# Performance work log

Hardware: AMD Instinct MI355X
Metric: run time of the kernel (lower is better)

Reference implementation:

```python
import jax, jax.numpy as jnp
import numpy as np

B, S, HID = 2, 2048, 2048
NH, NKV, HD = 16, 8, 128
EPS = 1e-6
THETA = 1e6
SCALE = HD ** -0.5


def setup_inputs() -> dict:
    key = jax.random.key(0)
    k0, k1, k2 = jax.random.split(key, 3)
    hidden_states = jax.random.normal(k0, (B, S, HID), dtype=jnp.float32) * 0.02
    # real RoPE tables (rotate-half convention, half-dim cos/sin)
    inv_freq = 1.0 / (THETA ** (jnp.arange(0, HD, 2, dtype=jnp.float32) / HD))
    freqs = jnp.outer(jnp.arange(S, dtype=jnp.float32), inv_freq)  # [S, HD//2]
    cos, sin = jnp.cos(freqs), jnp.sin(freqs)
    w_qkv = jax.random.normal(k1, ((NH + 2 * NKV) * HD, HID), dtype=jnp.float32) * 0.02
    q_norm_w = jnp.ones((HD,), dtype=jnp.float32)
    k_norm_w = jnp.ones((HD,), dtype=jnp.float32)
    w_o = jax.random.normal(k2, (HID, NH * HD), dtype=jnp.float32) * 0.02
    return {
        "hidden_states": hidden_states,
        "cos": cos,
        "sin": sin,
        "w_qkv": w_qkv,
        "q_norm_w": q_norm_w,
        "k_norm_w": k_norm_w,
        "w_o": w_o,
    }


def _rms_norm(x, w):
    # per-head RMSNorm over last dim (head_dim)
    var = jnp.mean(jnp.square(x), axis=-1, keepdims=True)
    return x * jax.lax.rsqrt(var + EPS) * w


def _rope(x, cos, sin):
    # x: [B, S, H, HD]; cos/sin: [S, HD//2]; rotate-half convention
    x1, x2 = x[..., : HD // 2], x[..., HD // 2 :]
    c = cos[None, :, None, :]
    s = sin[None, :, None, :]
    return jnp.concatenate([x1 * c - x2 * s, x2 * c + x1 * s], axis=-1)


def reference(hidden_states, cos, sin, w_qkv, q_norm_w, k_norm_w, w_o):
    # fused QKV projection
    qkv = jnp.einsum("bsh,oh->bso", hidden_states, w_qkv)
    q, k, v = jnp.split(qkv, [NH * HD, NH * HD + NKV * HD], axis=-1)
    q = q.reshape(B, S, NH, HD)
    k = k.reshape(B, S, NKV, HD)
    v = v.reshape(B, S, NKV, HD)
    # per-head QK RMSNorm, then RoPE
    q = _rope(_rms_norm(q, q_norm_w), cos, sin)
    k = _rope(_rms_norm(k, k_norm_w), cos, sin)
    # GQA: repeat KV heads across query groups
    groups = NH // NKV
    k = jnp.repeat(k, groups, axis=2)  # [B, S, NH, HD]
    v = jnp.repeat(v, groups, axis=2)
    # causal attention (prefill, full window)
    scores = jnp.einsum("bqhd,bkhd->bhqk", q, k) * SCALE
    causal = jnp.tril(jnp.ones((S, S), dtype=bool))
    scores = jnp.where(causal[None, None], scores, jnp.finfo(scores.dtype).min)
    probs = jax.nn.softmax(scores, axis=-1)
    attn = jnp.einsum("bhqk,bkhd->bqhd", probs, v).reshape(B, S, NH * HD)
    return jnp.einsum("bso,ho->bsh", attn, w_o)
```

## Files before the change

### kernel.cpp

```cpp
#include <hip/hip_runtime.h>
#include <stdint.h>
#include <stddef.h>

typedef __attribute__((ext_vector_type(8))) short bf16x8;
typedef __attribute__((ext_vector_type(4))) float f32x4;

#define B_ 2
#define S_ 2048
#define HID_ 2048
#define NH_ 16
#define NKV_ 8
#define HD_ 128
#define SCALE_ 0.08838834764831843f

__device__ __forceinline__ unsigned short f2bf(float f) {
  union { float f; unsigned int u; } v; v.f = f;
  unsigned int r = v.u + 0x7fffu + ((v.u >> 16) & 1u);
  return (unsigned short)(r >> 16);
}

__device__ __forceinline__ void gload16(const void* g, void* l) {
  __builtin_amdgcn_global_load_lds(
      (const __attribute__((address_space(1))) unsigned int*)g,
      (__attribute__((address_space(3))) unsigned int*)l, 16, 0, 0);
}

__global__ __launch_bounds__(256) void cvt_bf16(const float* __restrict__ src,
                                                unsigned short* __restrict__ dst,
                                                int n4) {
  int i = blockIdx.x * 256 + threadIdx.x;
  if (i < n4) {
    float4 v = ((const float4*)src)[i];
    ushort4 o;
    o.x = f2bf(v.x); o.y = f2bf(v.y); o.z = f2bf(v.z); o.w = f2bf(v.w);
    ((ushort4*)dst)[i] = o;
  }
}

__global__ __launch_bounds__(256) void gemm_bt(const unsigned short* __restrict__ A,
                                               const unsigned short* __restrict__ Bw,
                                               float* __restrict__ C,
                                               int M, int N, int K) {
  __shared__ __align__(16) char lds[32768];
  const int t = threadIdx.x, w = t >> 6, lane = t & 63;
  const int m0 = blockIdx.y * 128, n0 = blockIdx.x * 128;
  const int wr = w >> 1, wc = w & 1;
  const int l15 = lane & 15, l4 = lane >> 4;

  f32x4 acc[4][4];
#pragma unroll
  for (int i = 0; i < 4; ++i)
#pragma unroll
    for (int j = 0; j < 4; ++j) acc[i][j] = (f32x4){0.f, 0.f, 0.f, 0.f};

  const int nk = K >> 6;
  for (int kt = 0; kt < nk; ++kt) {
#pragma unroll
    for (int j = 0; j < 4; ++j) {
      int ob = ((w * 4 + j) << 10) + (lane << 4);
      int row = ob >> 7, inrow = ob & 127;
      int src = inrow ^ ((row & 7) << 4);
      gload16((const char*)A + ((size_t)(m0 + row) * K + kt * 64) * 2 + src,
              lds + ((w * 4 + j) << 10));
    }
#pragma unroll
    for (int j = 0; j < 4; ++j) {
      int ob = ((w * 4 + j) << 10) + (lane << 4);
      int row = ob >> 7, inrow = ob & 127;
      int src = inrow ^ ((row & 7) << 4);
      gload16((const char*)Bw + ((size_t)(n0 + row) * K + kt * 64) * 2 + src,
              lds + 16384 + ((w * 4 + j) << 10));
    }
    __syncthreads();
#pragma unroll
    for (int c = 0; c < 2; ++c) {
      bf16x8 af[4], bfr[4];
#pragma unroll
      for (int i = 0; i < 4; ++i) {
        int rowl = wr * 64 + i * 16 + l15;
        int inr = c * 64 + l4 * 16;
        af[i] = *(const bf16x8*)(lds + rowl * 128 + (inr ^ ((rowl & 7) << 4)));
      }
#pragma unroll
      for (int j = 0; j < 4; ++j) {
        int rowl = wc * 64 + j * 16 + l15;
        int inr = c * 64 + l4 * 16;
        bfr[j] = *(const bf16x8*)(lds + 16384 + rowl * 128 + (inr ^ ((rowl & 7) << 4)));
      }
#pragma unroll
      for (int i = 0; i < 4; ++i)
#pragma unroll
        for (int j = 0; j < 4; ++j)
          acc[i][j] = __builtin_amdgcn_mfma_f32_16x16x32_bf16(af[i], bfr[j], acc[i][j], 0, 0, 0);
    }
    __syncthreads();
  }
#pragma unroll
  for (int i = 0; i < 4; ++i)
#pragma unroll
    for (int j = 0; j < 4; ++j)
#pragma unroll
      for (int r = 0; r < 4; ++r) {
        int m = m0 + wr * 64 + i * 16 + l4 * 4 + r;
        int n = n0 + wc * 64 + j * 16 + l15;
        C[(size_t)m * N + n] = acc[i][j][r];
      }
}

__global__ __launch_bounds__(256) void norm_rope(const float* __restrict__ QKV,
                                                 const float* __restrict__ cosT,
                                                 const float* __restrict__ sinT,
                                                 const float* __restrict__ qw,
                                                 const float* __restrict__ kw,
                                                 unsigned short* __restrict__ qo,
                                                 unsigned short* __restrict__ ko) {
  int bs = blockIdx.x;
  int b = bs >> 11, s = bs & 2047;
  int t = threadIdx.x, hu = t >> 3, l8 = t & 7;
  if (hu >= 24) return;
  bool isq = hu < 16;
  int h = isq ? hu : hu - 16;
  const float* x = QKV + (size_t)bs * 4096 + (isq ? h * 128 : 2048 + h * 128);
  int d0 = l8 * 8;
  float x1[8] __attribute__((aligned(16)));
  float x2[8] __attribute__((aligned(16)));
  *(float4*)(x1) = *(const float4*)(x + d0);
  *(float4*)(x1 + 4) = *(const float4*)(x + d0 + 4);
  *(float4*)(x2) = *(const float4*)(x + d0 + 64);
  *(float4*)(x2 + 4) = *(const float4*)(x + d0 + 68);
  float ss = 0.f;
#pragma unroll
  for (int j = 0; j < 8; ++j) ss += x1[j] * x1[j] + x2[j] * x2[j];
  ss += __shfl_xor(ss, 1);
  ss += __shfl_xor(ss, 2);
  ss += __shfl_xor(ss, 4);
  float rstd = rsqrtf(ss * 0.0078125f + 1e-6f);
  const float* wn = isq ? qw : kw;
  float c[8] __attribute__((aligned(16)));
  float sn[8] __attribute__((aligned(16)));
  *(float4*)(c) = *(const float4*)(cosT + s * 64 + d0);
  *(float4*)(c + 4) = *(const float4*)(cosT + s * 64 + d0 + 4);
  *(float4*)(sn) = *(const float4*)(sinT + s * 64 + d0);
  *(float4*)(sn + 4) = *(const float4*)(sinT + s * 64 + d0 + 4);
  bf16x8 o1, o2;
#pragma unroll
  for (int j = 0; j < 8; ++j) {
    float a = x1[j] * rstd * wn[d0 + j];
    float bb = x2[j] * rstd * wn[d0 + 64 + j];
    o1[j] = (short)f2bf(a * c[j] - bb * sn[j]);
    o2[j] = (short)f2bf(bb * c[j] + a * sn[j]);
  }
  unsigned short* dst = isq ? qo + ((size_t)(b * 16 + h) * 2048 + s) * 128
                            : ko + ((size_t)(b * 8 + h) * 2048 + s) * 128;
  *(bf16x8*)(dst + d0) = o1;
  *(bf16x8*)(dst + d0 + 64) = o2;
}

__global__ __launch_bounds__(256) void transpose_v(const float* __restrict__ QKV,
                                                   unsigned short* __restrict__ vT) {
  __shared__ unsigned short tile[64][68];
  int bid = blockIdx.x;
  int hid = bid >> 6;
  int st = (bid >> 1) & 31, dt = bid & 1;
  int b = hid >> 3, hkv = hid & 7;
  int t = threadIdx.x;
#pragma unroll
  for (int i = 0; i < 16; ++i) {
    int idx = t + i * 256;
    int sl = idx >> 6, dl = idx & 63;
    float v = QKV[(size_t)(b * 2048 + st * 64 + sl) * 4096 + 3072 + hkv * 128 + dt * 64 + dl];
    tile[sl][dl] = f2bf(v);
  }
  __syncthreads();
#pragma unroll
  for (int i = 0; i < 16; ++i) {
    int idx = t + i * 256;
    int dl = idx >> 6, sl = idx & 63;
    vT[((size_t)(b * 8 + hkv) * 128 + dt * 64 + dl) * 2048 + st * 64 + sl] = tile[sl][dl];
  }
}

__global__ __launch_bounds__(256) void attn_fwd(const unsigned short* __restrict__ Q,
                                                const unsigned short* __restrict__ Kb,
                                                const unsigned short* __restrict__ Vt,
                                                unsigned short* __restrict__ Ao) {
  __shared__ __align__(16) char lds[74752];
  const int pr = blockIdx.x, h = blockIdx.y, b = blockIdx.z;
  const int hkv = h >> 1;
  const int t = threadIdx.x, w = t >> 6, lane = t & 63;
  const int l15 = lane & 15, l4 = lane >> 4;

  const unsigned short* Kg = Kb + ((size_t)(b * 8 + hkv) * 2048) * 128;
  const unsigned short* Vg = Vt + ((size_t)(b * 8 + hkv) * 128) * 2048;
  char* Pb = lds + 65536 + w * 2304;

  auto STAGE = [&](int bufi, int tt2) {
    char* kb = lds + bufi * 32768;
    char* vb = kb + 16384;
#pragma unroll
    for (int j = 0; j < 4; ++j) {
      int ob = ((w * 4 + j) << 10) + (lane << 4);
      int row = ob >> 8, inrow = ob & 255;
      int src = inrow ^ ((row & 7) << 4);
      gload16((const char*)(Kg + (size_t)tt2 * 64 * 128) + row * 256 + src,
              kb + ((w * 4 + j) << 10));
    }
#pragma unroll
    for (int j = 0; j < 4; ++j) {
      int ob = ((w * 4 + j) << 10) + (lane << 4);
      int row = ob >> 7, inrow = ob & 127;
      int src = inrow ^ ((row & 7) << 4);
      gload16((const char*)Vg + (size_t)row * 4096 + tt2 * 128 + src,
              vb + ((w * 4 + j) << 10));
    }
  };

  for (int hh = 0; hh < 2; ++hh) {
    const int qt = hh ? 31 - pr : pr;
    const int qrow0 = qt * 64;

    bf16x8 qf[4];
    const unsigned short* qp =
        Q + ((size_t)(b * 16 + h) * 2048 + qrow0 + w * 16 + l15) * 128;
#pragma unroll
    for (int c = 0; c < 4; ++c) qf[c] = *(const bf16x8*)(qp + c * 32 + l4 * 8);

    float mrow[4], lrow[4];
    f32x4 o[8];
#pragma unroll
    for (int r = 0; r < 4; ++r) { mrow[r] = -1e30f; lrow[r] = 0.f; }
#pragma unroll
    for (int dn = 0; dn < 8; ++dn) o[dn] = (f32x4){0.f, 0.f, 0.f, 0.f};

    int cur = 0;
    STAGE(0, 0);
    __syncthreads();

    for (int tt = 0; tt <= qt; ++tt) {
      if (tt < qt) STAGE(cur ^ 1, tt + 1);
      const char* kb = lds + cur * 32768;
      const char* vb = kb + 16384;

      f32x4 sacc[4];
#pragma unroll
      for (int n = 0; n < 4; ++n) sacc[n] = (f32x4){0.f, 0.f, 0.f, 0.f};
#pragma unroll
      for (int c = 0; c < 4; ++c) {
#pragma unroll
        for (int n = 0; n < 4; ++n) {
          int rowl = n * 16 + l15;
          int inr = c * 64 + l4 * 16;
          bf16x8 kf = *(const bf16x8*)(kb + rowl * 256 + (inr ^ ((rowl & 7) << 4)));
          sacc[n] = __builtin_amdgcn_mfma_f32_16x16x32_bf16(qf[c], kf, sacc[n], 0, 0, 0);
        }
      }

      float sc[4][4];
      bool diag = (tt == qt);
#pragma unroll
      for (int n = 0; n < 4; ++n)
#pragma unroll
        for (int r = 0; r < 4; ++r) {
          float v = sacc[n][r] * SCALE_;
          if (diag && (tt * 64 + n * 16 + l15 > qrow0 + w * 16 + l4 * 4 + r)) v = -1e30f;
          sc[n][r] = v;
        }
      float al[4];
#pragma unroll
      for (int r = 0; r < 4; ++r) {
        float tm = fmaxf(fmaxf(sc[0][r], sc[1][r]), fmaxf(sc[2][r], sc[3][r]));
        tm = fmaxf(tm, __shfl_xor(tm, 1));
        tm = fmaxf(tm, __shfl_xor(tm, 2));
        tm = fmaxf(tm, __shfl_xor(tm, 4));
        tm = fmaxf(tm, __shfl_xor(tm, 8));
        float mn = fmaxf(mrow[r], tm);
        al[r] = __expf(mrow[r] - mn);
        mrow[r] = mn;
      }
      float rs[4] = {0.f, 0.f, 0.f, 0.f};
#pragma unroll
      for (int n = 0; n < 4; ++n)
#pragma unroll
        for (int r = 0; r < 4; ++r) {
          float p = __expf(sc[n][r] - mrow[r]);
          sc[n][r] = p;
          rs[r] += p;
        }
#pragma unroll
      for (int r = 0; r < 4; ++r) {
        rs[r] += __shfl_xor(rs[r], 1);
        rs[r] += __shfl_xor(rs[r], 2);
        rs[r] += __shfl_xor(rs[r], 4);
        rs[r] += __shfl_xor(rs[r], 8);
        lrow[r] = lrow[r] * al[r] + rs[r];
      }
#pragma unroll
      for (int dn = 0; dn < 8; ++dn)
#pragma unroll
        for (int r = 0; r < 4; ++r) o[dn][r] *= al[r];

      unsigned short* Pp = (unsigned short*)Pb;
#pragma unroll
      for (int n = 0; n < 4; ++n)
#pragma unroll
        for (int r = 0; r < 4; ++r)
          Pp[(l4 * 4 + r) * 72 + n * 16 + l15] = f2bf(sc[n][r]);

#pragma unroll
      for (int c2 = 0; c2 < 2; ++c2) {
        bf16x8 pf = *(const bf16x8*)(Pb + l15 * 144 + c2 * 64 + l4 * 16);
#pragma unroll
        for (int dn = 0; dn < 8; ++dn) {
          int rowv = dn * 16 + l15;
          int inr = c2 * 64 + l4 * 16;
          bf16x8 vf = *(const bf16x8*)(vb + rowv * 128 + (inr ^ ((rowv & 7) << 4)));
          o[dn] = __builtin_amdgcn_mfma_f32_16x16x32_bf16(pf, vf, o[dn], 0, 0, 0);
        }
      }

      __syncthreads();
      cur ^= 1;
    }

#pragma unroll
    for (int r = 0; r < 4; ++r) {
      float inv = 1.f / lrow[r];
#pragma unroll
      for (int dn = 0; dn < 8; ++dn) {
        Ao[(size_t)(b * 2048 + qrow0 + w * 16 + l4 * 4 + r) * 2048 + h * 128 +
           dn * 16 + l15] = f2bf(o[dn][r] * inv);
      }
    }
  }
}

extern "C" void kernel_launch(void* const* d_in, const int* in_sizes, int n_in,
                              void* d_out, int out_size, void* d_ws, size_t ws_size,
                              hipStream_t stream) {
  const float* hidden = (const float*)d_in[0];
  const float* cosT = (const float*)d_in[1];
  const float* sinT = (const float*)d_in[2];
  const float* wqkv = (const float*)d_in[3];
  const float* qw = (const float*)d_in[4];
  const float* kw = (const float*)d_in[5];
  const float* wo = (const float*)d_in[6];
  float* out = (float*)d_out;
  char* ws = (char*)d_ws;

  unsigned short* Xb = (unsigned short*)(ws);
  unsigned short* Wqkvb = (unsigned short*)(ws + 16777216);
  unsigned short* Wob = (unsigned short*)(ws + 33554432);
  float* QKV = (float*)(ws + 41943040);
  unsigned short* Qb = (unsigned short*)(ws + 109051904);
  unsigned short* Kbuf = (unsigned short*)(ws + 125829120);
  unsigned short* VT = (unsigned short*)(ws + 134217728);
  unsigned short* An = (unsigned short*)(ws + 142606336);

  cvt_bf16<<<8192, 256, 0, stream>>>(hidden, Xb, 2097152);
  cvt_bf16<<<8192, 256, 0, stream>>>(wqkv, Wqkvb, 2097152);
  cvt_bf16<<<4096, 256, 0, stream>>>(wo, Wob, 1048576);

  gemm_bt<<<dim3(32, 32), 256, 0, stream>>>(Xb, Wqkvb, QKV, 4096, 4096, 2048);

  norm_rope<<<4096, 256, 0, stream>>>(QKV, cosT, sinT, qw, kw, Qb, Kbuf);
  transpose_v<<<1024, 256, 0, stream>>>(QKV, VT);

  attn_fwd<<<dim3(16, 16, 2), 256, 0, stream>>>(Qb, Kbuf, VT, An);

  gemm_bt<<<dim3(16, 32), 256, 0, stream>>>(An, Wob, out, 4096, 2048, 2048);
}
```

Baseline: 365.9 us.

## Use exp2 softmax with lazy rescaling, peel diagonal tile, add MFMA priority hints

The attention inner loop now folds log2(e) into the score scale so it can use exp2f. It skips rescaling the output accumulators and running sum unless a row max grows past a threshold, checked wave-wide. The diagonal causal tile is peeled into a separate compile-time-specialised call, so off-diagonal tiles carry no mask logic. s_setprio hints are wrapped around the MFMA sections. Lazy rescaling cuts per-tile VALU work but allows unnormalised exponents to reach about 2^11.5, which is a small numerical risk.

```diff
diff --git a/kernel.cpp b/kernel.cpp
--- a/kernel.cpp
+++ b/kernel.cpp
@@ -1,6 +1,7 @@
 #include <hip/hip_runtime.h>
 #include <stdint.h>
 #include <stddef.h>
+#include <type_traits>
 
 typedef __attribute__((ext_vector_type(8))) short bf16x8;
 typedef __attribute__((ext_vector_type(4))) float f32x4;
@@ -12,6 +13,8 @@
 #define NKV_ 8
 #define HD_ 128
 #define SCALE_ 0.08838834764831843f
+#define SCALE2_ 0.12751744978717884f
+#define THRL2_ 11.541560327111707f
 
 __device__ __forceinline__ unsigned short f2bf(float f) {
   union { float f; unsigned int u; } v; v.f = f;
@@ -233,17 +236,16 @@
     for (int dn = 0; dn < 8; ++dn) o[dn] = (f32x4){0.f, 0.f, 0.f, 0.f};
 
     int cur = 0;
-    STAGE(0, 0);
-    __syncthreads();
-
-    for (int tt = 0; tt <= qt; ++tt) {
-      if (tt < qt) STAGE(cur ^ 1, tt + 1);
+
+    auto tile_body = [&](int tt, auto diagc) {
+      constexpr bool DIAG = decltype(diagc)::value;
       const char* kb = lds + cur * 32768;
       const char* vb = kb + 16384;
 
       f32x4 sacc[4];
 #pragma unroll
       for (int n = 0; n < 4; ++n) sacc[n] = (f32x4){0.f, 0.f, 0.f, 0.f};
+      __builtin_amdgcn_s_setprio(1);
 #pragma unroll
       for (int c = 0; c < 4; ++c) {
 #pragma unroll
@@ -254,35 +256,46 @@
           sacc[n] = __builtin_amdgcn_mfma_f32_16x16x32_bf16(qf[c], kf, sacc[n], 0, 0, 0);
         }
       }
+      __builtin_amdgcn_s_setprio(0);
 
       float sc[4][4];
-      bool diag = (tt == qt);
 #pragma unroll
       for (int n = 0; n < 4; ++n)
 #pragma unroll
         for (int r = 0; r < 4; ++r) {
-          float v = sacc[n][r] * SCALE_;
-          if (diag && (tt * 64 + n * 16 + l15 > qrow0 + w * 16 + l4 * 4 + r)) v = -1e30f;
+          float v = sacc[n][r] * SCALE2_;
+          if (DIAG && (n * 16 + l15 > w * 16 + l4 * 4 + r)) v = -1e30f;
           sc[n][r] = v;
         }
-      float al[4];
+      float tm[4];
 #pragma unroll
       for (int r = 0; r < 4; ++r) {
-        float tm = fmaxf(fmaxf(sc[0][r], sc[1][r]), fmaxf(sc[2][r], sc[3][r]));
-        tm = fmaxf(tm, __shfl_xor(tm, 1));
-        tm = fmaxf(tm, __shfl_xor(tm, 2));
-        tm = fmaxf(tm, __shfl_xor(tm, 4));
-        tm = fmaxf(tm, __shfl_xor(tm, 8));
-        float mn = fmaxf(mrow[r], tm);
-        al[r] = __expf(mrow[r] - mn);
-        mrow[r] = mn;
+        float x = fmaxf(fmaxf(sc[0][r], sc[1][r]), fmaxf(sc[2][r], sc[3][r]));
+        x = fmaxf(x, __shfl_xor(x, 1));
+        x = fmaxf(x, __shfl_xor(x, 2));
+        x = fmaxf(x, __shfl_xor(x, 4));
+        x = fmaxf(x, __shfl_xor(x, 8));
+        tm[r] = x;
+      }
+      bool within = (tm[0] <= mrow[0] + THRL2_) & (tm[1] <= mrow[1] + THRL2_) &
+                    (tm[2] <= mrow[2] + THRL2_) & (tm[3] <= mrow[3] + THRL2_);
+      if (!__all(within)) {
+#pragma unroll
+        for (int r = 0; r < 4; ++r) {
+          float mn = fmaxf(mrow[r], tm[r]);
+          float al = exp2f(mrow[r] - mn);
+          mrow[r] = mn;
+          lrow[r] *= al;
+#pragma unroll
+          for (int dn = 0; dn < 8; ++dn) o[dn][r] *= al;
+        }
       }
       float rs[4] = {0.f, 0.f, 0.f, 0.f};
 #pragma unroll
       for (int n = 0; n < 4; ++n)
 #pragma unroll
         for (int r = 0; r < 4; ++r) {
-          float p = __expf(sc[n][r] - mrow[r]);
+          float p = exp2f(sc[n][r] - mrow[r]);
           sc[n][r] = p;
           rs[r] += p;
         }
@@ -292,12 +305,8 @@
         rs[r] += __shfl_xor(rs[r], 2);
         rs[r] += __shfl_xor(rs[r], 4);
         rs[r] += __shfl_xor(rs[r], 8);
-        lrow[r] = lrow[r] * al[r] + rs[r];
-      }
-#pragma unroll
-      for (int dn = 0; dn < 8; ++dn)
-#pragma unroll
-        for (int r = 0; r < 4; ++r) o[dn][r] *= al[r];
+        lrow[r] += rs[r];
+      }
 
       unsigned short* Pp = (unsigned short*)Pb;
 #pragma unroll
@@ -306,6 +315,7 @@
         for (int r = 0; r < 4; ++r)
           Pp[(l4 * 4 + r) * 72 + n * 16 + l15] = f2bf(sc[n][r]);
 
+      __builtin_amdgcn_s_setprio(1);
 #pragma unroll
       for (int c2 = 0; c2 < 2; ++c2) {
         bf16x8 pf = *(const bf16x8*)(Pb + l15 * 144 + c2 * 64 + l4 * 16);
@@ -317,10 +327,20 @@
           o[dn] = __builtin_amdgcn_mfma_f32_16x16x32_bf16(pf, vf, o[dn], 0, 0, 0);
         }
       }
-
+      __builtin_amdgcn_s_setprio(0);
+    };
+
+    STAGE(0, 0);
+    __syncthreads();
+
+    for (int tt = 0; tt < qt; ++tt) {
+      STAGE(cur ^ 1, tt + 1);
+      tile_body(tt, std::integral_constant<bool, false>{});
       __syncthreads();
       cur ^= 1;
     }
+    tile_body(qt, std::integral_constant<bool, true>{});
+    __syncthreads();
 
 #pragma unroll
     for (int r = 0; r < 4; ++r) {
```

Result: no change. 367.3 us (+0.4%).
